# Optimization experiments

Measured on AMD Instinct MI355X. Metric: run time of the kernel, lower is better.

## Reference

```python
import jax, jax.numpy as jnp
import numpy as np

B, T, D = 4, 4096, 1024

def setup_inputs() -> dict:
    key = jax.random.key(0)
    ks = jax.random.split(key, 7)
    s1 = 1.0 / np.sqrt(D)
    s2 = 1.0 / np.sqrt(2 * D)
    return {
        "x": jax.random.normal(ks[0], (B, T, D), jnp.float32),
        "W1": jax.random.uniform(ks[1], (D, 2 * D), jnp.float32, -s1, s1),      # Linear(D,2D,bias=False)
        "W2": jax.random.uniform(ks[2], (2 * D, 2 * D), jnp.float32, -s2, s2),  # Linear(2D,2D)
        "b2": jax.random.uniform(ks[3], (2 * D,), jnp.float32, -s2, s2),
        "conv_w": jax.random.uniform(ks[4], (D, 1, 3), jnp.float32, -1/np.sqrt(3), 1/np.sqrt(3)),  # depthwise k=3
        "gamma": jnp.ones((D,), jnp.float32),
        "beta": jnp.zeros((D,), jnp.float32),
    }

def _gated_scan(theta, alpha):
    # parallel stable scan: h_t = a_t * h_{t-1} + (1 - a_t) * tanh(theta_t), h_0 = 0
    a = jax.nn.sigmoid(alpha)
    b = (1.0 - a) * jnp.tanh(theta)
    def combine(c1, c2):
        a1, b1 = c1
        a2, b2 = c2
        return a1 * a2, a2 * b1 + b2
    _, h = jax.lax.associative_scan(combine, (a, b), axis=1)
    return h

def reference(x, W1, W2, b2, conv_w, gamma, beta):
    # morphism generator: Linear -> SiLU -> Linear
    mp = jax.nn.silu(x @ W1) @ W2 + b2                      # (B,T,2D)
    theta, alpha = jnp.split(mp, 2, axis=-1)
    semantic = _gated_scan(theta, alpha)                    # (B,T,D)
    # causal depthwise conv: left-pad 2, kernel 3, groups=D
    sc = jnp.transpose(semantic, (0, 2, 1))                 # (B,D,T)
    cb = jax.lax.conv_general_dilated(
        sc, conv_w, window_strides=(1,), padding=[(2, 0)],
        dimension_numbers=("NCH", "OIH", "NCH"), feature_group_count=D)
    cb = jax.nn.silu(jnp.transpose(cb, (0, 2, 1)))          # (B,T,D)
    y = semantic + 0.1 * cb
    # LayerNorm over D
    mu = jnp.mean(y, axis=-1, keepdims=True)
    var = jnp.mean(jnp.square(y - mu), axis=-1, keepdims=True)
    y = (y - mu) * jax.lax.rsqrt(var + 1e-5) * gamma + beta
    # dropout is identity in eval mode; L2 normalize (torch eps=1e-12)
    nrm = jnp.sqrt(jnp.sum(jnp.square(y), axis=-1, keepdims=True))
    return y / jnp.maximum(nrm, 1e-12)
```

## Files before the change

kernel.cpp:

```cpp
#include <hip/hip_runtime.h>
#include <cstdint>
#include <cstddef>

typedef __attribute__((ext_vector_type(8))) short bf16x8;
typedef __attribute__((ext_vector_type(4))) float f32x4;
typedef unsigned short u16;
typedef unsigned int u32;

__device__ __forceinline__ u16 f2bf(float f) {
  u32 u = __float_as_uint(f);
  u32 r = (u + 0x7fffu + ((u >> 16) & 1u)) >> 16;
  return (u16)r;
}
__device__ __forceinline__ float bf2f(u16 h) {
  return __uint_as_float(((u32)h) << 16);
}
__device__ __forceinline__ float fsilu(float v) { return v / (1.f + __expf(-v)); }
__device__ __forceinline__ float fsigmoid(float v) { return 1.f / (1.f + __expf(-v)); }

__device__ __forceinline__ void glds16(const void* g, void* l) {
  __builtin_amdgcn_global_load_lds(
      (const __attribute__((address_space(1))) void*)g,
      (__attribute__((address_space(3))) void*)l, 16, 0, 0);
}


__global__ __launch_bounds__(256) void cast_bf16_vec(const float* __restrict__ src,
                                                     u16* __restrict__ dst, int n4) {
  int i = blockIdx.x * 256 + threadIdx.x;
  if (i >= n4) return;
  const float4 v = ((const float4*)src)[i];
  ushort4 o;
  o.x = f2bf(v.x); o.y = f2bf(v.y); o.z = f2bf(v.z); o.w = f2bf(v.w);
  ((ushort4*)dst)[i] = o;
}

__global__ void transpose_cast(const float* __restrict__ src, u16* __restrict__ dst,
                               int R, int C) {
  __shared__ float tile[32][33];
  int bx = blockIdx.x * 32;
  int by = blockIdx.y * 32;
  int tx = threadIdx.x, ty = threadIdx.y;
#pragma unroll
  for (int i = 0; i < 4; ++i)
    tile[ty + i * 8][tx] = src[(size_t)(by + ty + i * 8) * C + bx + tx];
  __syncthreads();
#pragma unroll
  for (int i = 0; i < 4; ++i)
    dst[(size_t)(bx + ty + i * 8) * R + by + tx] = f2bf(tile[tx][ty + i * 8]);
}


template <int EPI>
__global__ __launch_bounds__(256, 2) void gemm_bt(const u16* __restrict__ A,
                                                  const u16* __restrict__ Bt,
                                                  u16* __restrict__ C,
                                                  const float* __restrict__ bias,
                                                  int M, int N, int K) {
  __shared__ u16 lA[128 * 32];
  __shared__ u16 lB[128 * 32];
  const int tid = threadIdx.x;
  const int lane = tid & 63;
  const int wid = tid >> 6;
  const int wr = wid >> 1, wc = wid & 1;
  const long bm = (long)blockIdx.y * 128;
  const long bn = (long)blockIdx.x * 128;

  f32x4 acc[4][4] = {};

  const int srow = tid >> 2;
  const int skoff = (tid & 3) * 8;
  const u16* gA = A + (bm + srow) * (long)K + skoff;
  const u16* gB = Bt + (bn + srow) * (long)K + skoff;
  u16* lA0 = &lA[srow * 32 + skoff];
  u16* lA1 = &lA[(64 + srow) * 32 + skoff];
  u16* lB0 = &lB[srow * 32 + skoff];
  u16* lB1 = &lB[(64 + srow) * 32 + skoff];

  const int fr = lane & 15;
  const int fk = (lane >> 4) * 8;
  const u16* pA = &lA[(wr * 64 + fr) * 32 + fk];
  const u16* pB = &lB[(wc * 64 + fr) * 32 + fk];

  for (int kk = 0; kk < K; kk += 32) {
    glds16(gA + kk, lA0);
    glds16(gA + 64 * (long)K + kk, lA1);
    glds16(gB + kk, lB0);
    glds16(gB + 64 * (long)K + kk, lB1);
    __syncthreads();
    bf16x8 af[4], bf[4];
#pragma unroll
    for (int m = 0; m < 4; ++m) af[m] = *(const bf16x8*)(pA + m * 16 * 32);
#pragma unroll
    for (int n = 0; n < 4; ++n) bf[n] = *(const bf16x8*)(pB + n * 16 * 32);
#pragma unroll
    for (int m = 0; m < 4; ++m)
#pragma unroll
      for (int n = 0; n < 4; ++n)
        acc[m][n] =
            __builtin_amdgcn_mfma_f32_16x16x32_bf16(af[m], bf[n], acc[m][n], 0, 0, 0);
    __syncthreads();
  }

  const int erow0 = (lane >> 4) * 4;
  const int ecol = lane & 15;
#pragma unroll
  for (int m = 0; m < 4; ++m) {
#pragma unroll
    for (int n = 0; n < 4; ++n) {
#pragma unroll
      for (int j = 0; j < 4; ++j) {
        long row = bm + wr * 64 + m * 16 + erow0 + j;
        long col = bn + wc * 64 + n * 16 + ecol;
        float v = acc[m][n][j];
        if (EPI == 0) {
          v = fsilu(v);
        } else {
          v += bias[col];
          v = (col < 1024) ? tanhf(v) : fsigmoid(v);
        }
        C[row * (long)N + col] = f2bf(v);
      }
    }
  }
}


__global__ __launch_bounds__(256) void scan_stage1(const u16* __restrict__ sa,
                                                   float* __restrict__ cA,
                                                   float* __restrict__ cB) {
  const int tid = blockIdx.x * 256 + threadIdx.x;
  const int d = tid & 1023;
  const int chunk = (tid >> 10) & 63;
  const int b = tid >> 16;
  const size_t base = ((size_t)(b * 4096 + chunk * 64)) * 2048 + d;
  float Ac = 1.f, Bc = 0.f;
#pragma unroll 4
  for (int t = 0; t < 64; ++t) {
    float s = bf2f(sa[base + (size_t)t * 2048]);
    float a = bf2f(sa[base + (size_t)t * 2048 + 1024]);
    Bc = a * Bc + (1.f - a) * s;
    Ac *= a;
  }
  cA[tid] = Ac;
  cB[tid] = Bc;
}

__global__ __launch_bounds__(256) void scan_stage2(const float* __restrict__ cA,
                                                   const float* __restrict__ cB,
                                                   float* __restrict__ hstart) {
  const int tid = blockIdx.x * 256 + threadIdx.x;
  const int d = tid & 1023;
  const int b = tid >> 10;
  float h = 0.f;
  for (int c = 0; c < 64; ++c) {
    const size_t i = ((size_t)(b * 64 + c)) * 1024 + d;
    hstart[i] = h;
    h = cA[i] * h + cB[i];
  }
}

__global__ __launch_bounds__(256) void scan_stage3(const u16* __restrict__ sa,
                                                   const float* __restrict__ hstart,
                                                   float* __restrict__ sem) {
  const int tid = blockIdx.x * 256 + threadIdx.x;
  const int d = tid & 1023;
  const int chunk = (tid >> 10) & 63;
  const int b = tid >> 16;
  const size_t m0 = (size_t)(b * 4096 + chunk * 64);
  const size_t base = m0 * 2048 + d;
  float h = hstart[tid];
#pragma unroll 4
  for (int t = 0; t < 64; ++t) {
    float s = bf2f(sa[base + (size_t)t * 2048]);
    float a = bf2f(sa[base + (size_t)t * 2048 + 1024]);
    h = a * h + (1.f - a) * s;
    sem[(m0 + t) * 1024 + d] = h;
  }
}


__global__ __launch_bounds__(256) void finalize(const float* __restrict__ sem,
                                                const float* __restrict__ cw,
                                                const float* __restrict__ gamma,
                                                const float* __restrict__ beta,
                                                float* __restrict__ out) {
  const int r = blockIdx.x;
  const int t = r & 4095;
  const int tid = threadIdx.x;
  const int lane = tid & 63, wid = tid >> 6;
  const int d0 = tid * 4;
  const float4 zero = make_float4(0.f, 0.f, 0.f, 0.f);
  float4 s0 = ((const float4*)(sem + (size_t)r * 1024))[tid];
  float4 s1 = (t >= 1) ? ((const float4*)(sem + (size_t)(r - 1) * 1024))[tid] : zero;
  float4 s2 = (t >= 2) ? ((const float4*)(sem + (size_t)(r - 2) * 1024))[tid] : zero;
  float a0[4] = {s0.x, s0.y, s0.z, s0.w};
  float a1[4] = {s1.x, s1.y, s1.z, s1.w};
  float a2[4] = {s2.x, s2.y, s2.z, s2.w};
  float y[4];
  float vs = 0.f, vq = 0.f;
#pragma unroll
  for (int j = 0; j < 4; ++j) {
    int d = d0 + j;
    float cb = cw[d * 3] * a2[j] + cw[d * 3 + 1] * a1[j] + cw[d * 3 + 2] * a0[j];
    cb = fsilu(cb);
    y[j] = a0[j] + 0.1f * cb;
    vs += y[j];
    vq += y[j] * y[j];
  }
  __shared__ float rb[2][4];
#pragma unroll
  for (int o = 32; o > 0; o >>= 1) {
    vs += __shfl_down(vs, o);
    vq += __shfl_down(vq, o);
  }
  if (lane == 0) { rb[0][wid] = vs; rb[1][wid] = vq; }
  __syncthreads();
  float tsum = rb[0][0] + rb[0][1] + rb[0][2] + rb[0][3];
  float tss = rb[1][0] + rb[1][1] + rb[1][2] + rb[1][3];
  float mu = tsum * (1.f / 1024.f);
  float var = tss * (1.f / 1024.f) - mu * mu;
  float rstd = rsqrtf(var + 1e-5f);
  float yn[4];
  float q = 0.f;
#pragma unroll
  for (int j = 0; j < 4; ++j) {
    int d = d0 + j;
    yn[j] = (y[j] - mu) * rstd * gamma[d] + beta[d];
    q += yn[j] * yn[j];
  }
#pragma unroll
  for (int o = 32; o > 0; o >>= 1) q += __shfl_down(q, o);
  __syncthreads();
  if (lane == 0) rb[0][wid] = q;
  __syncthreads();
  float nrm = sqrtf(rb[0][0] + rb[0][1] + rb[0][2] + rb[0][3]);
  float scale = 1.f / fmaxf(nrm, 1e-12f);
  float4 o4 = make_float4(yn[0] * scale, yn[1] * scale, yn[2] * scale, yn[3] * scale);
  ((float4*)(out + (size_t)r * 1024))[tid] = o4;
}


extern "C" void kernel_launch(void* const* d_in, const int* in_sizes, int n_in,
                              void* d_out, int out_size, void* d_ws, size_t ws_size,
                              hipStream_t stream) {
  const float* x = (const float*)d_in[0];
  const float* W1 = (const float*)d_in[1];
  const float* W2 = (const float*)d_in[2];
  const float* b2 = (const float*)d_in[3];
  const float* cw = (const float*)d_in[4];
  const float* gamma = (const float*)d_in[5];
  const float* beta = (const float*)d_in[6];
  float* out = (float*)d_out;
  char* ws = (char*)d_ws;

  u16* xb = (u16*)(ws);
  u16* w1t = (u16*)(ws + 33554432);
  u16* w2t = (u16*)(ws + 37748736);
  u16* h1 = (u16*)(ws + 46137344);
  float* sem = (float*)(ws + 46137344);
  u16* sa = (u16*)(ws + 113246208);
  float* cA = (float*)(ws);
  float* cB = (float*)(ws + 1048576);
  float* hstart = (float*)(ws + 2097152);

  cast_bf16_vec<<<16384, 256, 0, stream>>>(x, xb, 4194304);
  transpose_cast<<<dim3(64, 32), dim3(32, 8), 0, stream>>>(W1, w1t, 1024, 2048);
  transpose_cast<<<dim3(64, 64), dim3(32, 8), 0, stream>>>(W2, w2t, 2048, 2048);
  gemm_bt<0><<<dim3(16, 128), 256, 0, stream>>>(xb, w1t, h1, nullptr, 16384, 2048, 1024);
  gemm_bt<1><<<dim3(16, 128), 256, 0, stream>>>(h1, w2t, sa, b2, 16384, 2048, 2048);
  scan_stage1<<<1024, 256, 0, stream>>>(sa, cA, cB);
  scan_stage2<<<16, 256, 0, stream>>>(cA, cB, hstart);
  scan_stage3<<<1024, 256, 0, stream>>>(sa, hstart, sem);
  finalize<<<16384, 256, 0, stream>>>(sem, cw, gamma, beta, out);
}
```

Baseline: 373.2 us.

## Replace GEMM with 256x256 tile, double-buffered LDS pipeline and swizzled layout

Replaces the 128x128 single-buffered bf16 GEMM with a 256x256-tile, 512-thread kernel that uses K=64 steps. LDS is double-buffered, global-to-LDS loads are interleaved across four MFMA phases, the LDS layout is XOR-swizzled to avoid bank conflicts, and the block order is swizzled for L2 locality. The aim is to raise arithmetic intensity and overlap memory with MFMA work in both GEMMs, which dominate runtime. The price is 128KB of LDS per block and hand-written waitcnt/barrier scheduling that is fragile. With 128KB of LDS per block, likely only one block fits per CU despite the launch bound of 2.

```diff
diff --git a/kernel.cpp b/kernel.cpp
--- a/kernel.cpp
+++ b/kernel.cpp
@@ -23,6 +23,12 @@
       (const __attribute__((address_space(1))) void*)g,
       (__attribute__((address_space(3))) void*)l, 16, 0, 0);
 }
+
+#define FENCE_MEM() asm volatile("" ::: "memory")
+#define BAR() __builtin_amdgcn_s_barrier()
+#define VMCNT(n) asm volatile("s_waitcnt vmcnt(" #n ")" ::: "memory")
+#define LGKM0() asm volatile("s_waitcnt lgkmcnt(0)" ::: "memory")
+#define SFENCE() __builtin_amdgcn_sched_barrier(0)
 
 
 __global__ __launch_bounds__(256) void cast_bf16_vec(const float* __restrict__ src,
@@ -52,77 +58,148 @@
 
 
 template <int EPI>
-__global__ __launch_bounds__(256, 2) void gemm_bt(const u16* __restrict__ A,
+__global__ __launch_bounds__(512, 2) void gemm256(const u16* __restrict__ A,
                                                   const u16* __restrict__ Bt,
-                                                  u16* __restrict__ C,
+                                                  u16* __restrict__ Co,
                                                   const float* __restrict__ bias,
                                                   int M, int N, int K) {
-  __shared__ u16 lA[128 * 32];
-  __shared__ u16 lB[128 * 32];
+  __shared__ char lds[131072];
   const int tid = threadIdx.x;
   const int lane = tid & 63;
   const int wid = tid >> 6;
-  const int wr = wid >> 1, wc = wid & 1;
-  const long bm = (long)blockIdx.y * 128;
-  const long bn = (long)blockIdx.x * 128;
-
-  f32x4 acc[4][4] = {};
-
-  const int srow = tid >> 2;
-  const int skoff = (tid & 3) * 8;
-  const u16* gA = A + (bm + srow) * (long)K + skoff;
-  const u16* gB = Bt + (bn + srow) * (long)K + skoff;
-  u16* lA0 = &lA[srow * 32 + skoff];
-  u16* lA1 = &lA[(64 + srow) * 32 + skoff];
-  u16* lB0 = &lB[srow * 32 + skoff];
-  u16* lB1 = &lB[(64 + srow) * 32 + skoff];
-
-  const int fr = lane & 15;
-  const int fk = (lane >> 4) * 8;
-  const u16* pA = &lA[(wr * 64 + fr) * 32 + fk];
-  const u16* pB = &lB[(wc * 64 + fr) * 32 + fk];
-
-  for (int kk = 0; kk < K; kk += 32) {
-    glds16(gA + kk, lA0);
-    glds16(gA + 64 * (long)K + kk, lA1);
-    glds16(gB + kk, lB0);
-    glds16(gB + 64 * (long)K + kk, lB1);
-    __syncthreads();
-    bf16x8 af[4], bf[4];
-#pragma unroll
-    for (int m = 0; m < 4; ++m) af[m] = *(const bf16x8*)(pA + m * 16 * 32);
-#pragma unroll
-    for (int n = 0; n < 4; ++n) bf[n] = *(const bf16x8*)(pB + n * 16 * 32);
-#pragma unroll
-    for (int m = 0; m < 4; ++m)
-#pragma unroll
-      for (int n = 0; n < 4; ++n)
-        acc[m][n] =
-            __builtin_amdgcn_mfma_f32_16x16x32_bf16(af[m], bf[n], acc[m][n], 0, 0, 0);
-    __syncthreads();
-  }
-
-  const int erow0 = (lane >> 4) * 4;
+  const int wr = wid >> 2;
+  const int wc = wid & 3;
+
+  const int gx = gridDim.x;
+  const int nwg = gx * gridDim.y;
+  const int bid = blockIdx.y * gx + blockIdx.x;
+  const int swz = (bid & 7) * (nwg >> 3) + (bid >> 3);
+  const long bm = (long)(swz / gx) * 256;
+  const long bn = (long)(swz % gx) * 256;
+
+  const int NT = K >> 6;
+
+  const int r0 = tid >> 3, c0p = tid & 7;
+  const int r1 = r0 + 64;
+  const int gA0 = (r0 & 63) + ((r0 >> 6) << 7);
+  const int gA1 = (r1 & 63) + ((r1 >> 6) << 7);
+  const int gB0 = (r0 & 31) + ((r0 >> 5) << 6);
+  const int gB1 = (r1 & 31) + ((r1 >> 5) << 6);
+  const int cA0 = c0p ^ (r0 & 7);
+  const size_t srcA0 = (size_t)(bm + gA0) * K + cA0 * 8;
+  const size_t srcA1 = (size_t)(bm + gA1) * K + cA0 * 8;
+  const size_t srcB0 = (size_t)(bn + gB0) * K + cA0 * 8;
+  const size_t srcB1 = (size_t)(bn + gB1) * K + cA0 * 8;
+  const int dstA0 = gA0 * 128 + c0p * 16;
+  const int dstA1 = gA1 * 128 + c0p * 16;
+  const int dstB0 = 32768 + gB0 * 128 + c0p * 16;
+  const int dstB1 = 32768 + gB1 * 128 + c0p * 16;
+  const size_t halfA = (size_t)64 * K;
+  const size_t halfB = (size_t)32 * K;
+
+#define STAGE_A(buf, half, t)                                                        \
+  do {                                                                               \
+    glds16(A + srcA0 + (half) * halfA + (size_t)(t) * 64,                            \
+           lds + (buf) * 65536 + dstA0 + (half) * 8192);                             \
+    glds16(A + srcA1 + (half) * halfA + (size_t)(t) * 64,                            \
+           lds + (buf) * 65536 + dstA1 + (half) * 8192);                             \
+  } while (0)
+#define STAGE_B(buf, half, t)                                                        \
+  do {                                                                               \
+    glds16(Bt + srcB0 + (half) * halfB + (size_t)(t) * 64,                           \
+           lds + (buf) * 65536 + dstB0 + (half) * 4096);                             \
+    glds16(Bt + srcB1 + (half) * halfB + (size_t)(t) * 64,                           \
+           lds + (buf) * 65536 + dstB1 + (half) * 4096);                             \
+  } while (0)
+
+  const int l15 = lane & 15, l3 = lane & 7, g4 = lane >> 4;
+  const int aoff0 = (wr * 128 + l15) * 128 + ((g4 ^ l3) * 16);
+  const int aoff1 = (wr * 128 + l15) * 128 + (((4 + g4) ^ l3) * 16);
+  const int boff0 = 32768 + (wc * 64 + l15) * 128 + ((g4 ^ l3) * 16);
+  const int boff1 = 32768 + (wc * 64 + l15) * 128 + (((4 + g4) ^ l3) * 16);
+
+  f32x4 acc[8][4] = {};
+
+#define PHASE(buf, qm, qn, STMT, TAIL)                                               \
+  do {                                                                               \
+    bf16x8 af[4][2], bfr[2][2];                                                      \
+    const char* base = lds + (buf) * 65536;                                          \
+    _Pragma("unroll") for (int mm = 0; mm < 4; ++mm) {                               \
+      af[mm][0] = *(const bf16x8*)(base + aoff0 + ((qm) * 4 + mm) * 2048);           \
+      af[mm][1] = *(const bf16x8*)(base + aoff1 + ((qm) * 4 + mm) * 2048);           \
+    }                                                                                \
+    _Pragma("unroll") for (int nn = 0; nn < 2; ++nn) {                               \
+      bfr[nn][0] = *(const bf16x8*)(base + boff0 + ((qn) * 2 + nn) * 2048);          \
+      bfr[nn][1] = *(const bf16x8*)(base + boff1 + ((qn) * 2 + nn) * 2048);          \
+    }                                                                                \
+    STMT;                                                                            \
+    FENCE_MEM();                                                                     \
+    BAR();                                                                           \
+    LGKM0();                                                                         \
+    SFENCE();                                                                        \
+    __builtin_amdgcn_s_setprio(1);                                                   \
+    _Pragma("unroll") for (int mm = 0; mm < 4; ++mm)                                 \
+        _Pragma("unroll") for (int nn = 0; nn < 2; ++nn) {                           \
+      acc[(qm) * 4 + mm][(qn) * 2 + nn] = __builtin_amdgcn_mfma_f32_16x16x32_bf16(   \
+          af[mm][0], bfr[nn][0], acc[(qm) * 4 + mm][(qn) * 2 + nn], 0, 0, 0);        \
+      acc[(qm) * 4 + mm][(qn) * 2 + nn] = __builtin_amdgcn_mfma_f32_16x16x32_bf16(   \
+          af[mm][1], bfr[nn][1], acc[(qm) * 4 + mm][(qn) * 2 + nn], 0, 0, 0);        \
+    }                                                                                \
+    __builtin_amdgcn_s_setprio(0);                                                   \
+    TAIL;                                                                            \
+    BAR();                                                                           \
+    FENCE_MEM();                                                                     \
+  } while (0)
+
+  STAGE_A(0, 0, 0);
+  STAGE_A(0, 1, 0);
+  STAGE_B(0, 0, 0);
+  STAGE_B(0, 1, 0);
+  FENCE_MEM();
+  if (NT > 1) {
+    STAGE_A(1, 0, 1);
+    STAGE_B(1, 0, 1);
+  }
+  VMCNT(4);
+  BAR();
+  FENCE_MEM();
+
+  for (int t = 0; t < NT; ++t) {
+    const int p = t & 1;
+    const bool s1 = (t + 1) < NT;
+    const bool s2 = (t + 2) < NT;
+    PHASE(p, 0, 0, { if (s1) STAGE_A(p ^ 1, 1, t + 1); }, {});
+    PHASE(p, 0, 1, { if (s1) STAGE_B(p ^ 1, 1, t + 1); }, {});
+    PHASE(p, 1, 0, { if (s2) STAGE_A(p, 0, t + 2); }, {});
+    PHASE(p, 1, 1, { if (s2) STAGE_B(p, 0, t + 2); },
+          { if (s2) { VMCNT(4); } else { VMCNT(0); } });
+  }
+
+  const int erow = (lane >> 4) * 4;
   const int ecol = lane & 15;
 #pragma unroll
-  for (int m = 0; m < 4; ++m) {
-#pragma unroll
-    for (int n = 0; n < 4; ++n) {
+  for (int mf = 0; mf < 8; ++mf) {
+#pragma unroll
+    for (int nf = 0; nf < 4; ++nf) {
+      const long col = bn + wc * 64 + nf * 16 + ecol;
+      float badd = (EPI == 1) ? bias[col] : 0.f;
 #pragma unroll
       for (int j = 0; j < 4; ++j) {
-        long row = bm + wr * 64 + m * 16 + erow0 + j;
-        long col = bn + wc * 64 + n * 16 + ecol;
-        float v = acc[m][n][j];
+        const long row = bm + wr * 128 + mf * 16 + erow + j;
+        float v = acc[mf][nf][j];
         if (EPI == 0) {
           v = fsilu(v);
         } else {
-          v += bias[col];
+          v += badd;
           v = (col < 1024) ? tanhf(v) : fsigmoid(v);
         }
-        C[row * (long)N + col] = f2bf(v);
+        Co[row * (long)N + col] = f2bf(v);
       }
     }
   }
+#undef STAGE_A
+#undef STAGE_B
+#undef PHASE
 }
 
 
@@ -267,8 +344,8 @@
   cast_bf16_vec<<<16384, 256, 0, stream>>>(x, xb, 4194304);
   transpose_cast<<<dim3(64, 32), dim3(32, 8), 0, stream>>>(W1, w1t, 1024, 2048);
   transpose_cast<<<dim3(64, 64), dim3(32, 8), 0, stream>>>(W2, w2t, 2048, 2048);
-  gemm_bt<0><<<dim3(16, 128), 256, 0, stream>>>(xb, w1t, h1, nullptr, 16384, 2048, 1024);
-  gemm_bt<1><<<dim3(16, 128), 256, 0, stream>>>(h1, w2t, sa, b2, 16384, 2048, 2048);
+  gemm256<0><<<dim3(8, 64), 512, 0, stream>>>(xb, w1t, h1, nullptr, 16384, 2048, 1024);
+  gemm256<1><<<dim3(8, 64), 512, 0, stream>>>(h1, w2t, sa, b2, 16384, 2048, 2048);
   scan_stage1<<<1024, 256, 0, stream>>>(sa, cA, cB);
   scan_stage2<<<16, 256, 0, stream>>>(cA, cB, hstart);
   scan_stage3<<<1024, 256, 0, stream>>>(sa, hstart, sem);
```

Result: no change. 373.4 us (+0.0%).
